# Optimization experiments

Measured on AMD Instinct MI355X. Metric: run time of the kernel, lower is better.

The kernel has to match this reference:

```python
import jax, jax.numpy as jnp
import numpy as np


def _base_grid(H, W, dtype):
    # pixel-center grid in [-1, 1], matching get_base_grid
    gy = (jnp.arange(H, dtype=dtype) + 0.5) * (2.0 / H) - 1.0  # [H]
    gx = (jnp.arange(W, dtype=dtype) + 0.5) * (2.0 / W) - 1.0  # [W]
    return gy, gx


def _bilinear_sample(img, grid):
    # img: [N, C, H, W]; grid: [N, H, W, 2] in [-1,1] (x, y)
    # matches F.grid_sample(mode='bilinear', padding_mode='zeros', align_corners=False)
    N, C, H, W = img.shape
    ix = (grid[..., 0] + 1.0) * 0.5 * W - 0.5  # [N,H,W]
    iy = (grid[..., 1] + 1.0) * 0.5 * H - 0.5
    x0 = jnp.floor(ix)
    y0 = jnp.floor(iy)
    wx1 = ix - x0
    wy1 = iy - y0
    wx0 = 1.0 - wx1
    wy0 = 1.0 - wy1
    x0i = x0.astype(jnp.int32)
    y0i = y0.astype(jnp.int32)
    img_flat = img.reshape(N, C, H * W)

    def gather(xi, yi):
        valid = (xi >= 0) & (xi < W) & (yi >= 0) & (yi < H)  # zeros padding
        xc = jnp.clip(xi, 0, W - 1)
        yc = jnp.clip(yi, 0, H - 1)
        idx = (yc * W + xc).reshape(N, 1, H * W)
        v = jnp.take_along_axis(img_flat, idx, axis=2).reshape(N, C, H, W)
        return v * valid[:, None, :, :].astype(img.dtype)

    v00 = gather(x0i, y0i)
    v01 = gather(x0i + 1, y0i)
    v10 = gather(x0i, y0i + 1)
    v11 = gather(x0i + 1, y0i + 1)
    w00 = (wy0 * wx0)[:, None]
    w01 = (wy0 * wx1)[:, None]
    w10 = (wy1 * wx0)[:, None]
    w11 = (wy1 * wx1)[:, None]
    return v00 * w00 + v01 * w01 + v10 * w10 + v11 * w11


def _warp_grid(flow, wrap_x=True):
    # flow: [N, 2, H, W] -> grid [N, H, W, 2]
    N, _, H, W = flow.shape
    gy, gx = _base_grid(H, W, flow.dtype)
    fx = gx[None, None, :] + flow[:, 0]  # [N,H,W]
    fy = gy[None, :, None] + flow[:, 1]
    if wrap_x:
        fx = jnp.remainder(fx + 1.0, 2.0) - 1.0
    return jnp.stack([fx, fy], axis=-1)


def _pscan(flows, images, wrap_x=True):
    B, L, _, H, W = flows.shape
    C = images.shape[2]
    step = 1
    while step < L:
        fp = flows[:, :-step].reshape(-1, 2, H, W)
        ip = images[:, :-step].reshape(-1, C, H, W)
        fc = flows[:, step:].reshape(-1, 2, H, W)
        ic = images[:, step:].reshape(-1, C, H, W)
        grid = _warp_grid(fc, wrap_x=wrap_x)
        nf = fc + _bilinear_sample(fp, grid)
        ni = ic + _bilinear_sample(ip, grid)
        flows = jnp.concatenate(
            [flows[:, :step], nf.reshape(B, L - step, 2, H, W)], axis=1)
        images = jnp.concatenate(
            [images[:, :step], ni.reshape(B, L - step, C, H, W)], axis=1)
        step *= 2
    return images


def setup_inputs() -> dict:
    key = jax.random.key(0)
    k1, k2 = jax.random.split(key)
    B, L, C, H, W = 4, 32, 16, 192, 192
    flows = jax.random.normal(k1, (B, L, 2, H, W), dtype=jnp.float32) * 0.05
    images = jax.random.normal(k2, (B, L, C, H, W), dtype=jnp.float32)
    return {"flows": flows, "images": images}


def reference(flows, images):
    return _pscan(flows, images, wrap_x=True)
```

## Files before the change

### kernel.cpp

```cpp
#include <hip/hip_runtime.h>

#define BB 4
#define LL 32
#define CC 16
#define HH 192
#define WW 192
#define HW (HH * WW)
#define CHW (CC * HW)
#define IMG_ELEMS ((size_t)BB * LL * CHW)
#define FLW_ELEMS ((size_t)BB * LL * 2 * HW)
#define TILES 144
#define NXCD 8

__device__ __forceinline__ const float* sel3(int u, int shalf,
                                             const float* pin,
                                             const float* pa,
                                             const float* pb) {
  int q = (u > 0) ? (1 << (31 - __builtin_clz((unsigned)u))) : 0;
  q = q < shalf ? q : shalf;
  if (q == 0) return pin;
  return (q == 1 || q == 4) ? pa : pb;
}

__global__ __launch_bounds__(256) void pscan_step(
    const float* __restrict__ img_in, const float* __restrict__ img_b0,
    const float* __restrict__ img_out_r,
    const float* __restrict__ flow_in, const float* __restrict__ flow_b0,
    const float* __restrict__ flow_b1,
    float* __restrict__ img_dst, float* __restrict__ flow_dst,
    int s, int write_flow, int pairs_per_xcd, int total_pairs, int ntt) {
#pragma clang fp contract(off)
  const int l = blockIdx.x;
  const int xcd = l & (NXCD - 1);
  const int j = l >> 3;
  const int pair = xcd * pairs_per_xcd + j / TILES;
  if (pair >= total_pairs) return;
  const int tile = j % TILES;
  const int b = pair / ntt;
  const int t = pair % ntt + s;
  const int u = t - s;
  const int w = (tile % 3) * 64 + threadIdx.x;
  const int h = (tile / 3) * 4 + threadIdx.y;
  const int shalf = s >> 1;

  const float* fcur = sel3(t, shalf, flow_in, flow_b0, flow_b1);
  const float* fprv = sel3(u, shalf, flow_in, flow_b0, flow_b1);
  const float* icur = sel3(t, shalf, img_in, img_b0, img_out_r);
  const float* iprv = sel3(u, shalf, img_in, img_b0, img_out_r);

  const int p = h * WW + w;

  const size_t fcbase = ((size_t)(b * LL + t) * 2) * HW;
  const float fcx = __builtin_nontemporal_load(fcur + fcbase + p);
  const float fcy = __builtin_nontemporal_load(fcur + fcbase + HW + p);

  const float gx = (w + 0.5f) * (2.0f / WW) - 1.0f;
  const float gy = (h + 0.5f) * (2.0f / HH) - 1.0f;
  float fx = gx + fcx;
  float fy = gy + fcy;
  float r = fmodf(fx + 1.0f, 2.0f);
  if (r < 0.0f) r += 2.0f;
  fx = r - 1.0f;

  const float ix = (fx + 1.0f) * 0.5f * WW - 0.5f;
  const float iy = (fy + 1.0f) * 0.5f * HH - 0.5f;
  const float x0f = floorf(ix), y0f = floorf(iy);
  const float wx1 = ix - x0f, wy1 = iy - y0f;
  const float wx0 = 1.0f - wx1, wy0 = 1.0f - wy1;
  const int x0 = (int)x0f, y0 = (int)y0f;
  const int x1 = x0 + 1, y1 = y0 + 1;
  const bool vx0 = (x0 >= 0) & (x0 < WW), vx1 = (x1 >= 0) & (x1 < WW);
  const bool vy0 = (y0 >= 0) & (y0 < HH), vy1 = (y1 >= 0) & (y1 < HH);
  const int cx0 = min(max(x0, 0), WW - 1), cx1 = min(max(x1, 0), WW - 1);
  const int cy0 = min(max(y0, 0), HH - 1), cy1 = min(max(y1, 0), HH - 1);
  const float w00 = wy0 * wx0 * ((vy0 && vx0) ? 1.0f : 0.0f);
  const float w01 = wy0 * wx1 * ((vy0 && vx1) ? 1.0f : 0.0f);
  const float w10 = wy1 * wx0 * ((vy1 && vx0) ? 1.0f : 0.0f);
  const float w11 = wy1 * wx1 * ((vy1 && vx1) ? 1.0f : 0.0f);
  const int i00 = cy0 * WW + cx0, i01 = cy0 * WW + cx1;
  const int i10 = cy1 * WW + cx0, i11 = cy1 * WW + cx1;

  if (write_flow) {
    const float* fp0 = fprv + ((size_t)(b * LL + u) * 2) * HW;
    const float* fp1 = fp0 + HW;
    const float s0 = w00 * fp0[i00] + w01 * fp0[i01] + w10 * fp0[i10] + w11 * fp0[i11];
    const float s1 = w00 * fp1[i00] + w01 * fp1[i01] + w10 * fp1[i10] + w11 * fp1[i11];
    __builtin_nontemporal_store(fcx + s0, flow_dst + fcbase + p);
    __builtin_nontemporal_store(fcy + s1, flow_dst + fcbase + HW + p);
  }

  const float* ip = iprv + (size_t)(b * LL + u) * CHW;
  const float* ic = icur + (size_t)(b * LL + t) * CHW;
  float* od = img_dst + (size_t)(b * LL + t) * CHW;
#pragma unroll 4
  for (int c = 0; c < CC; ++c) {
    const float* pl = ip + c * HW;
    const float sv = w00 * pl[i00] + w01 * pl[i01] + w10 * pl[i10] + w11 * pl[i11];
    const float cv = __builtin_nontemporal_load(ic + c * HW + p);
    __builtin_nontemporal_store(cv + sv, od + c * HW + p);
  }
}

__global__ __launch_bounds__(256) void pscan_fixup(
    const float* __restrict__ img_in, const float* __restrict__ img_b0,
    float* __restrict__ img_out) {
  const int per_slice4 = (int)(BB * CHW / 4);
  int tid = blockIdx.x * blockDim.x + threadIdx.x;
  int j = tid / per_slice4;
  if (j >= 6) return;
  int e = tid % per_slice4;
  const int t = (j == 0) ? 0 : (j == 1 ? 1 : j + 2);
  const float* src = (j == 0) ? img_in : img_b0;
  const int b = e / (CHW / 4);
  const int rr = e % (CHW / 4);
  const size_t base = (size_t)(b * LL + t) * CHW;
  const float4* s4 = (const float4*)(src + base) + rr;
  float4* d4 = (float4*)(img_out + base) + rr;
  *d4 = *s4;
}

extern "C" void kernel_launch(void* const* d_in, const int* in_sizes, int n_in,
                              void* d_out, int out_size, void* d_ws, size_t ws_size,
                              hipStream_t stream) {
  const float* flow_in = (const float*)d_in[0];
  const float* img_in  = (const float*)d_in[1];
  float* img_out = (float*)d_out;

  float* img_b0  = (float*)d_ws;
  float* flow_b0 = img_b0 + IMG_ELEMS;
  float* flow_b1 = flow_b0 + FLW_ELEMS;

  const dim3 blk(64, 4, 1);
  const int steps[5] = {1, 2, 4, 8, 16};
  for (int i = 0; i < 5; ++i) {
    const int s = steps[i];
    const int ntt = LL - s;
    const int total_pairs = BB * ntt;
    const int ppx = (total_pairs + NXCD - 1) / NXCD;
    const dim3 grd((unsigned)(NXCD * ppx * TILES), 1, 1);
    float* idst = (s == 1 || s == 4) ? img_b0 : img_out;
    float* fdst = (s == 1 || s == 4) ? flow_b0 : flow_b1;
    pscan_step<<<grd, blk, 0, stream>>>(img_in, img_b0, img_out,
                                        flow_in, flow_b0, flow_b1,
                                        idst, fdst, s, (s < 16) ? 1 : 0,
                                        ppx, total_pairs, ntt);
  }
  const int total4 = 6 * BB * CHW / 4;
  pscan_fixup<<<(total4 + 255) / 256, 256, 0, stream>>>(img_in, img_b0, img_out);
}
```

Baseline: 2.790 ms.

## Switch pscan intermediates to channel-last layout with vectorized bilinear gathers

Adds a pre-pass that converts images and flows from NCHW to NHWC (channel-interleaved) workspace buffers. Each scan step then gathers four corners as contiguous float4 vectors of 16 channels, instead of 16 scattered scalar loads per corner across channel planes. The last step writes NCHW directly, and fixup kernels transpose the untouched slices back. The cost is an extra full transpose pass, a second full-size image workspace buffer, and strided scalar stores in the final step.

Result: faster. 2.706 ms (-3.0%).

```diff
diff --git a/kernel.cpp b/kernel.cpp
--- a/kernel.cpp
+++ b/kernel.cpp
@@ -7,28 +7,51 @@
 #define WW 192
 #define HW (HH * WW)
 #define CHW (CC * HW)
+#define FHW (2 * HW)
 #define IMG_ELEMS ((size_t)BB * LL * CHW)
-#define FLW_ELEMS ((size_t)BB * LL * 2 * HW)
+#define FLW_ELEMS ((size_t)BB * LL * FHW)
 #define TILES 144
 #define NXCD 8
 
-__device__ __forceinline__ const float* sel3(int u, int shalf,
-                                             const float* pin,
-                                             const float* pa,
-                                             const float* pb) {
+typedef float f4v __attribute__((ext_vector_type(4)));
+typedef float f2v __attribute__((ext_vector_type(2)));
+
+__device__ __forceinline__ bool useB_sel(int u, int shalf) {
   int q = (u > 0) ? (1 << (31 - __builtin_clz((unsigned)u))) : 0;
   q = q < shalf ? q : shalf;
-  if (q == 0) return pin;
-  return (q == 1 || q == 4) ? pa : pb;
-}
-
-__global__ __launch_bounds__(256) void pscan_step(
-    const float* __restrict__ img_in, const float* __restrict__ img_b0,
-    const float* __restrict__ img_out_r,
-    const float* __restrict__ flow_in, const float* __restrict__ flow_b0,
-    const float* __restrict__ flow_b1,
+  return (q == 1 || q == 4);
+}
+
+__global__ __launch_bounds__(256) void conv_nhwc(
+    const float* __restrict__ img_in, const float* __restrict__ flow_in,
+    float* __restrict__ img_a, float* __restrict__ flow_a) {
+  const int b = blockIdx.z, t = blockIdx.y, tile = blockIdx.x;
+  const int w = (tile % 3) * 64 + threadIdx.x;
+  const int h = (tile / 3) * 4 + threadIdx.y;
+  const int p = h * WW + w;
+  const size_t ib = (size_t)(b * LL + t) * CHW;
+  float v[CC];
+#pragma unroll
+  for (int c = 0; c < CC; ++c)
+    v[c] = __builtin_nontemporal_load(img_in + ib + c * HW + p);
+  f4v* d = (f4v*)(img_a + ib + (size_t)p * CC);
+#pragma unroll
+  for (int k = 0; k < 4; ++k) {
+    f4v x = {v[4 * k], v[4 * k + 1], v[4 * k + 2], v[4 * k + 3]};
+    __builtin_nontemporal_store(x, d + k);
+  }
+  const size_t fb = (size_t)(b * LL + t) * FHW;
+  f2v f = {__builtin_nontemporal_load(flow_in + fb + p),
+           __builtin_nontemporal_load(flow_in + fb + HW + p)};
+  __builtin_nontemporal_store(f, (f2v*)(flow_a + fb + 2 * p));
+}
+
+__global__ __launch_bounds__(256) void pscan_step_nhwc(
+    const float* __restrict__ img_a, const float* __restrict__ img_b,
+    const float* __restrict__ flow_a, const float* __restrict__ flow_b,
     float* __restrict__ img_dst, float* __restrict__ flow_dst,
-    int s, int write_flow, int pairs_per_xcd, int total_pairs, int ntt) {
+    int s, int write_flow, int final_nchw,
+    int pairs_per_xcd, int total_pairs, int ntt) {
 #pragma clang fp contract(off)
   const int l = blockIdx.x;
   const int xcd = l & (NXCD - 1);
@@ -43,16 +66,17 @@
   const int h = (tile / 3) * 4 + threadIdx.y;
   const int shalf = s >> 1;
 
-  const float* fcur = sel3(t, shalf, flow_in, flow_b0, flow_b1);
-  const float* fprv = sel3(u, shalf, flow_in, flow_b0, flow_b1);
-  const float* icur = sel3(t, shalf, img_in, img_b0, img_out_r);
-  const float* iprv = sel3(u, shalf, img_in, img_b0, img_out_r);
+  const bool curB = useB_sel(t, shalf), prvB = useB_sel(u, shalf);
+  const float* fcur = curB ? flow_b : flow_a;
+  const float* fprv = prvB ? flow_b : flow_a;
+  const float* icur = curB ? img_b : img_a;
+  const float* iprv = prvB ? img_b : img_a;
 
   const int p = h * WW + w;
 
-  const size_t fcbase = ((size_t)(b * LL + t) * 2) * HW;
-  const float fcx = __builtin_nontemporal_load(fcur + fcbase + p);
-  const float fcy = __builtin_nontemporal_load(fcur + fcbase + HW + p);
+  const size_t fcb = (size_t)(b * LL + t) * FHW;
+  const f2v fc = __builtin_nontemporal_load((const f2v*)(fcur + fcb + 2 * p));
+  const float fcx = fc.x, fcy = fc.y;
 
   const float gx = (w + 0.5f) * (2.0f / WW) - 1.0f;
   const float gy = (h + 0.5f) * (2.0f / HH) - 1.0f;
@@ -81,42 +105,90 @@
   const int i10 = cy1 * WW + cx0, i11 = cy1 * WW + cx1;
 
   if (write_flow) {
-    const float* fp0 = fprv + ((size_t)(b * LL + u) * 2) * HW;
-    const float* fp1 = fp0 + HW;
-    const float s0 = w00 * fp0[i00] + w01 * fp0[i01] + w10 * fp0[i10] + w11 * fp0[i11];
-    const float s1 = w00 * fp1[i00] + w01 * fp1[i01] + w10 * fp1[i10] + w11 * fp1[i11];
-    __builtin_nontemporal_store(fcx + s0, flow_dst + fcbase + p);
-    __builtin_nontemporal_store(fcy + s1, flow_dst + fcbase + HW + p);
-  }
-
-  const float* ip = iprv + (size_t)(b * LL + u) * CHW;
-  const float* ic = icur + (size_t)(b * LL + t) * CHW;
-  float* od = img_dst + (size_t)(b * LL + t) * CHW;
-#pragma unroll 4
-  for (int c = 0; c < CC; ++c) {
-    const float* pl = ip + c * HW;
-    const float sv = w00 * pl[i00] + w01 * pl[i01] + w10 * pl[i10] + w11 * pl[i11];
-    const float cv = __builtin_nontemporal_load(ic + c * HW + p);
-    __builtin_nontemporal_store(cv + sv, od + c * HW + p);
-  }
-}
-
-__global__ __launch_bounds__(256) void pscan_fixup(
-    const float* __restrict__ img_in, const float* __restrict__ img_b0,
-    float* __restrict__ img_out) {
-  const int per_slice4 = (int)(BB * CHW / 4);
-  int tid = blockIdx.x * blockDim.x + threadIdx.x;
-  int j = tid / per_slice4;
-  if (j >= 6) return;
-  int e = tid % per_slice4;
-  const int t = (j == 0) ? 0 : (j == 1 ? 1 : j + 2);
-  const float* src = (j == 0) ? img_in : img_b0;
-  const int b = e / (CHW / 4);
-  const int rr = e % (CHW / 4);
+    const float* fpb = fprv + (size_t)(b * LL + u) * FHW;
+    const f2v g00 = *(const f2v*)(fpb + 2 * i00);
+    const f2v g01 = *(const f2v*)(fpb + 2 * i01);
+    const f2v g10 = *(const f2v*)(fpb + 2 * i10);
+    const f2v g11 = *(const f2v*)(fpb + 2 * i11);
+    const float s0 = w00 * g00.x + w01 * g01.x + w10 * g10.x + w11 * g11.x;
+    const float s1 = w00 * g00.y + w01 * g01.y + w10 * g10.y + w11 * g11.y;
+    f2v o = {fcx + s0, fcy + s1};
+    __builtin_nontemporal_store(o, (f2v*)(flow_dst + fcb + 2 * p));
+  }
+
+  const float* ipb = iprv + (size_t)(b * LL + u) * CHW;
+  const f4v* t00 = (const f4v*)(ipb + (size_t)i00 * CC);
+  const f4v* t01 = (const f4v*)(ipb + (size_t)i01 * CC);
+  const f4v* t10 = (const f4v*)(ipb + (size_t)i10 * CC);
+  const f4v* t11 = (const f4v*)(ipb + (size_t)i11 * CC);
+  const f4v* icp = (const f4v*)(icur + (size_t)(b * LL + t) * CHW + (size_t)p * CC);
+
+  if (!final_nchw) {
+    f4v* odp = (f4v*)(img_dst + (size_t)(b * LL + t) * CHW + (size_t)p * CC);
+#pragma unroll
+    for (int k = 0; k < 4; ++k) {
+      const f4v a = t00[k], e = t01[k], c = t10[k], d = t11[k];
+      const f4v cv = __builtin_nontemporal_load(icp + k);
+      f4v o;
+      {
+        const float s0 = w00 * a.x + w01 * e.x + w10 * c.x + w11 * d.x;
+        const float s1 = w00 * a.y + w01 * e.y + w10 * c.y + w11 * d.y;
+        const float s2 = w00 * a.z + w01 * e.z + w10 * c.z + w11 * d.z;
+        const float s3 = w00 * a.w + w01 * e.w + w10 * c.w + w11 * d.w;
+        o.x = cv.x + s0; o.y = cv.y + s1; o.z = cv.z + s2; o.w = cv.w + s3;
+      }
+      __builtin_nontemporal_store(o, odp + k);
+    }
+  } else {
+    float* od = img_dst + (size_t)(b * LL + t) * CHW;
+#pragma unroll
+    for (int k = 0; k < 4; ++k) {
+      const f4v a = t00[k], e = t01[k], c = t10[k], d = t11[k];
+      const f4v cv = __builtin_nontemporal_load(icp + k);
+      const float s0 = w00 * a.x + w01 * e.x + w10 * c.x + w11 * d.x;
+      const float s1 = w00 * a.y + w01 * e.y + w10 * c.y + w11 * d.y;
+      const float s2 = w00 * a.z + w01 * e.z + w10 * c.z + w11 * d.z;
+      const float s3 = w00 * a.w + w01 * e.w + w10 * c.w + w11 * d.w;
+      __builtin_nontemporal_store(cv.x + s0, od + (4 * k + 0) * HW + p);
+      __builtin_nontemporal_store(cv.y + s1, od + (4 * k + 1) * HW + p);
+      __builtin_nontemporal_store(cv.z + s2, od + (4 * k + 2) * HW + p);
+      __builtin_nontemporal_store(cv.w + s3, od + (4 * k + 3) * HW + p);
+    }
+  }
+}
+
+__global__ __launch_bounds__(256) void fixup_t0(const float* __restrict__ img_in,
+                                                float* __restrict__ img_out) {
+  const int per_b = CHW / 4;
+  int idx = blockIdx.x * blockDim.x + threadIdx.x;
+  if (idx >= BB * per_b) return;
+  const int b = idx / per_b, rr = idx % per_b;
+  const size_t base = (size_t)(b * LL) * CHW;
+  ((f4v*)(img_out + base))[rr] = ((const f4v*)(img_in + base))[rr];
+}
+
+__global__ __launch_bounds__(256) void fixup_tr(const float* __restrict__ img_a,
+                                                const float* __restrict__ img_b,
+                                                float* __restrict__ img_out) {
+  const int b = blockIdx.z;
+  const int t = blockIdx.y + 1;
+  const int tile = blockIdx.x;
+  const int w = (tile % 3) * 64 + threadIdx.x;
+  const int h = (tile / 3) * 4 + threadIdx.y;
+  const int p = h * WW + w;
+  const bool useB = (t == 1) || (t >= 4 && t < 8);
+  const float* src = useB ? img_b : img_a;
   const size_t base = (size_t)(b * LL + t) * CHW;
-  const float4* s4 = (const float4*)(src + base) + rr;
-  float4* d4 = (float4*)(img_out + base) + rr;
-  *d4 = *s4;
+  const f4v* sp = (const f4v*)(src + base + (size_t)p * CC);
+  float* od = img_out + base;
+#pragma unroll
+  for (int k = 0; k < 4; ++k) {
+    const f4v v = __builtin_nontemporal_load(sp + k);
+    __builtin_nontemporal_store(v.x, od + (4 * k + 0) * HW + p);
+    __builtin_nontemporal_store(v.y, od + (4 * k + 1) * HW + p);
+    __builtin_nontemporal_store(v.z, od + (4 * k + 2) * HW + p);
+    __builtin_nontemporal_store(v.w, od + (4 * k + 3) * HW + p);
+  }
 }
 
 extern "C" void kernel_launch(void* const* d_in, const int* in_sizes, int n_in,
@@ -126,11 +198,14 @@
   const float* img_in  = (const float*)d_in[1];
   float* img_out = (float*)d_out;
 
-  float* img_b0  = (float*)d_ws;
-  float* flow_b0 = img_b0 + IMG_ELEMS;
-  float* flow_b1 = flow_b0 + FLW_ELEMS;
+  float* img_a  = (float*)d_ws;
+  float* img_b  = img_a + IMG_ELEMS;
+  float* flow_a = img_b + IMG_ELEMS;
+  float* flow_b = flow_a + FLW_ELEMS;
 
   const dim3 blk(64, 4, 1);
+  conv_nhwc<<<dim3(TILES, LL, BB), blk, 0, stream>>>(img_in, flow_in, img_a, flow_a);
+
   const int steps[5] = {1, 2, 4, 8, 16};
   for (int i = 0; i < 5; ++i) {
     const int s = steps[i];
@@ -138,13 +213,13 @@
     const int total_pairs = BB * ntt;
     const int ppx = (total_pairs + NXCD - 1) / NXCD;
     const dim3 grd((unsigned)(NXCD * ppx * TILES), 1, 1);
-    float* idst = (s == 1 || s == 4) ? img_b0 : img_out;
-    float* fdst = (s == 1 || s == 4) ? flow_b0 : flow_b1;
-    pscan_step<<<grd, blk, 0, stream>>>(img_in, img_b0, img_out,
-                                        flow_in, flow_b0, flow_b1,
-                                        idst, fdst, s, (s < 16) ? 1 : 0,
-                                        ppx, total_pairs, ntt);
-  }
-  const int total4 = 6 * BB * CHW / 4;
-  pscan_fixup<<<(total4 + 255) / 256, 256, 0, stream>>>(img_in, img_b0, img_out);
-}
+    float* idst = (s == 16) ? img_out : ((s == 1 || s == 4) ? img_b : img_a);
+    float* fdst = (s == 1 || s == 4) ? flow_b : flow_a;
+    pscan_step_nhwc<<<grd, blk, 0, stream>>>(img_a, img_b, flow_a, flow_b,
+                                             idst, fdst, s, (s < 16) ? 1 : 0,
+                                             (s == 16) ? 1 : 0,
+                                             ppx, total_pairs, ntt);
+  }
+  fixup_t0<<<(BB * (CHW / 4) + 255) / 256, 256, 0, stream>>>(img_in, img_out);
+  fixup_tr<<<dim3(TILES, 15, BB), blk, 0, stream>>>(img_a, img_b, img_out);
+}
```
